# Kernel tuning notes

Hardware: AMD Instinct MI355X
Metric: run time of the kernel (lower is better)

The kernel has to match this reference:

```python
import jax, jax.numpy as jnp
import numpy as np

N_GROUPS = 4


def setup_inputs() -> dict:
    key = jax.random.key(0)
    ks = jax.random.split(key, 6)
    I, J, B = 512, 512, 4  # query tokens, key tokens, grid batch (B = 1 * n_groups)
    n_dim, out_per_group = 128, 4  # n_heads // n_groups = 16 // 4
    grid_q = jax.random.normal(ks[0], (I, 3), dtype=jnp.float32)
    grid_kv = jax.random.normal(ks[1], (B, J, 3), dtype=jnp.float32)
    W1 = jax.random.normal(ks[2], (3, n_dim), dtype=jnp.float32) * (1.0 / np.sqrt(3))
    b1 = jnp.zeros((n_dim,), dtype=jnp.float32)
    W2 = jax.random.normal(ks[3], (n_dim, n_dim), dtype=jnp.float32) * (1.0 / np.sqrt(n_dim))
    b2 = jnp.zeros((n_dim,), dtype=jnp.float32)
    W3 = jax.random.normal(ks[4], (n_dim, out_per_group), dtype=jnp.float32) * (1.0 / np.sqrt(n_dim))
    b3 = jnp.zeros((out_per_group,), dtype=jnp.float32)
    return {"grid_q": grid_q, "grid_kv": grid_kv, "W1": W1, "b1": b1,
            "W2": W2, "b2": b2, "W3": W3, "b3": b3}


def reference(grid_q, grid_kv, W1, b1, W2, b2, W3, b3):
    # grid_q: [I, 3] -> [1, I, 3]; grid_kv: [B, J, 3]
    gq = grid_q[None, :, :]
    # pairwise position difference: [B, I, J, 3]
    pos = gq[:, :, None, :] - grid_kv[:, None, :, :]
    # sign-log transform
    bias = jnp.sign(pos) * jnp.log1p(jnp.abs(pos))
    # tiny MLP: 3 -> n_dim -> n_dim -> heads//groups, pointwise over (B, I, J)
    h = jax.nn.relu(jnp.einsum('bijc,cd->bijd', bias, W1) + b1)
    h = jax.nn.relu(jnp.einsum('bijd,de->bije', h, W2) + b2)
    out = jnp.einsum('bije,eo->bijo', h, W3) + b3  # [B, I, J, O]
    # rearrange '(b g) i j o -> b (g o) i j' with g = N_GROUPS
    B, I, J, O = out.shape
    out = out.reshape(B // N_GROUPS, N_GROUPS, I, J, O)
    out = jnp.transpose(out, (0, 1, 4, 2, 3)).reshape(B // N_GROUPS, N_GROUPS * O, I, J)
    return out
```

## Files before the change

kernel.cpp:

```cpp
#include <hip/hip_runtime.h>
#include <math.h>

#define NDIM 128
#define TILE 64
#define NBLOCKS 1024
#define THREADS 512
#define POS_PER_BLOCK 1024
#define ITERS 16
#define CH 512

typedef __attribute__((ext_vector_type(8)))  short  short8;
typedef __attribute__((ext_vector_type(16))) float  float16;

__device__ __forceinline__ unsigned cvt_pk(float lo, float hi) {
    unsigned r;
    asm("v_cvt_pk_bf16_f32 %0, %1, %2" : "=v"(r) : "v"(lo), "v"(hi));
    return r;
}

__device__ __forceinline__ int kmap(int c, int jj) {
    return 32 * (c >> 2) + 16 * ((c >> 1) & 1) + 4 * (c & 1) + ((jj >> 2) << 3) + (jj & 3);
}

__global__ __launch_bounds__(512, 4)
void crpb_mfma7(const float* __restrict__ gq,
                const float* __restrict__ gkv,
                const float* __restrict__ W1,
                const float* __restrict__ b1,
                const float* __restrict__ W2,
                const float* __restrict__ b2,
                const float* __restrict__ W3,
                const float* __restrict__ b3,
                float* __restrict__ out)
{
    __shared__ __align__(16) unsigned short ash[2][16 * CH];
    __shared__ __align__(16) float red[2][4 * 4 * 64];

    const int tid  = threadIdx.x;
    const int lane = tid & 63;
    const int w    = __builtin_amdgcn_readfirstlane(tid >> 6);
    const int l31  = lane & 31;
    const int lh   = lane >> 5;

    const int ct = w & 3;
    const int ph = w >> 2;

    float16 b1cv, b2cv;
    #pragma unroll
    for (int q = 0; q < 16; ++q) {
        const int row = (q & 3) + 8 * (q >> 2) + 4 * lh;
        b1cv[q] = b1[ct * 32 + row];
        b2cv[q] = b2[ct * 32 + row];
    }

    short8 w1f;
    {
        const int ch = ct * 32 + l31;
        const float w0 = W1[ch], w1v = W1[128 + ch], w2v = W1[256 + ch];
        const unsigned u0 = cvt_pk(w0, w0), u1 = cvt_pk(w1v, w1v), u2 = cvt_pk(w2v, w2v);
        const float w0h = __uint_as_float(u0 << 16);
        const float w1h = __uint_as_float(u1 << 16);
        const float w2h = __uint_as_float(u2 << 16);
        const float w0l = w0 - w0h, w1l = w1v - w1h, w2l = w2v - w2h;
        unsigned d[4];
        if (lh == 0) {
            d[0] = cvt_pk(w0h, w0l);
            d[1] = cvt_pk(w0h, w1h);
            d[2] = cvt_pk(w1l, w1h);
            d[3] = cvt_pk(w2h, w2l);
        } else {
            d[0] = cvt_pk(w2h, 0.0f);
            d[1] = 0; d[2] = 0; d[3] = 0;
        }
        __builtin_memcpy(&w1f, d, 16);
    }

    short8 a2f[8];
    #pragma unroll
    for (int ks = 0; ks < 8; ++ks) {
        const int c = 2 * ks + lh;
        unsigned t0[4];
        #pragma unroll
        for (int t = 0; t < 4; ++t) {
            const int d0 = kmap(c, 2 * t), d1 = d0 + 1;
            t0[t] = cvt_pk(W2[d0 * 128 + ct * 32 + l31], W2[d1 * 128 + ct * 32 + l31]);
        }
        __builtin_memcpy(&a2f[ks], t0, 16);
    }

    short8 w3a[2];
    #pragma unroll
    for (int m = 0; m < 2; ++m) {
        unsigned tt[4];
        #pragma unroll
        for (int t = 0; t < 4; ++t) {
            const int chl = ((2 * t) & 3) + 8 * ((2 * t) >> 2) + 4 * lh + 16 * m;
            const int ch0 = ct * 32 + chl, ch1 = ch0 + 1;
            const float lo = (l31 < 4) ? W3[ch0 * 4 + l31] : 0.0f;
            const float hi = (l31 < 4) ? W3[ch1 * 4 + l31] : 0.0f;
            tt[t] = cvt_pk(lo, hi);
        }
        __builtin_memcpy(&w3a[m], tt, 16);
    }
    const float b3r = b3[(tid >> 6) & 3];

    const int posblock = blockIdx.x * POS_PER_BLOCK;
    const int bb = posblock >> 18;
    const float* kvrow = gkv + (size_t)(bb << 9) * 3;

    int ii = (posblock >> 9) & 511;
    float q0 = gq[ii * 3 + 0], q1 = gq[ii * 3 + 1], q2 = gq[ii * 3 + 2];
    const int pofs = ph * 32 + l31;
    const float* kp = kvrow + (size_t)((posblock & 511) + pofs) * 3;
    float kv0 = kp[0], kv1 = kp[1], kv2 = kp[2];

    auto phaseA = [&](int x, int buf) {
        const float c0 = q0 - kv0, c1 = q1 - kv1, c2 = q2 - kv2;
        const int pn = posblock + (((x + 1) & 15) << 6);
        const int iN = (pn >> 9) & 511, jN = pn & 511;
        q0 = gq[iN * 3 + 0]; q1 = gq[iN * 3 + 1]; q2 = gq[iN * 3 + 2];
        const float* kn = kvrow + (size_t)(jN + pofs) * 3;
        kv0 = kn[0]; kv1 = kn[1]; kv2 = kn[2];

        const float f0 = copysignf(__logf(1.0f + fabsf(c0)), c0);
        const float f1 = copysignf(__logf(1.0f + fabsf(c1)), c1);
        const float f2 = copysignf(__logf(1.0f + fabsf(c2)), c2);

        const unsigned u0 = cvt_pk(f0, f0), u1 = cvt_pk(f1, f1), u2 = cvt_pk(f2, f2);
        const float f0h = __uint_as_float(u0 << 16);
        const float f1h = __uint_as_float(u1 << 16);
        const float f2h = __uint_as_float(u2 << 16);
        const float f0l = f0 - f0h, f1l = f1 - f1h, f2l = f2 - f2h;

        unsigned d[4];
        if (lh == 0) {
            d[0] = u0;
            d[1] = cvt_pk(f0l, f1);
            d[2] = cvt_pk(f1, f1l);
            d[3] = u2;
        } else {
            d[0] = cvt_pk(f2l, 0.0f);
            d[1] = 0; d[2] = 0; d[3] = 0;
        }
        short8 bf; __builtin_memcpy(&bf, d, 16);

        float16 c1r = __builtin_amdgcn_mfma_f32_32x32x16_bf16(w1f, bf, b1cv, 0, 0, 0);

        unsigned pk0[4], pk1[4];
        #pragma unroll
        for (int t = 0; t < 4; ++t) {
            pk0[t] = cvt_pk(fmaxf(c1r[2 * t], 0.f),     fmaxf(c1r[2 * t + 1], 0.f));
            pk1[t] = cvt_pk(fmaxf(c1r[8 + 2 * t], 0.f), fmaxf(c1r[8 + 2 * t + 1], 0.f));
        }
        short8 v0, v1;
        __builtin_memcpy(&v0, pk0, 16);
        __builtin_memcpy(&v1, pk1, 16);
        *(short8*)&ash[buf][(4 * ct + lh) * CH + pofs * 8]     = v0;
        *(short8*)&ash[buf][(4 * ct + 2 + lh) * CH + pofs * 8] = v1;
    };

    phaseA(0, 0);
    __syncthreads();

    for (int it = 0; it < ITERS; ++it) {
        const int buf = it & 1;
        const int posbase = posblock + it * TILE;
        const int i  = (posbase >> 9) & 511;
        const int jb = posbase & 511;

        const unsigned short* br = &ash[buf][lh * CH + (ph * 32 + l31) * 8];
        short8 bfrag0 = *(const short8*)(br);
        float16 acc = __builtin_amdgcn_mfma_f32_32x32x16_bf16(a2f[0], bfrag0, b2cv, 0, 0, 0);
        #pragma unroll
        for (int ks = 1; ks < 8; ++ks) {
            short8 bfrag = *(const short8*)(br + ks * 2 * CH);
            acc = __builtin_amdgcn_mfma_f32_32x32x16_bf16(a2f[ks], bfrag, acc, 0, 0, 0);
        }

        {
            unsigned pk0[4], pk1[4];
            #pragma unroll
            for (int t = 0; t < 4; ++t) {
                pk0[t] = cvt_pk(fmaxf(acc[2 * t], 0.f),     fmaxf(acc[2 * t + 1], 0.f));
                pk1[t] = cvt_pk(fmaxf(acc[8 + 2 * t], 0.f), fmaxf(acc[8 + 2 * t + 1], 0.f));
            }
            short8 bm0, bm1;
            __builtin_memcpy(&bm0, pk0, 16);
            __builtin_memcpy(&bm1, pk1, 16);
            float16 p;
            #pragma unroll
            for (int r = 0; r < 16; ++r) p[r] = 0.0f;
            p = __builtin_amdgcn_mfma_f32_32x32x16_bf16(w3a[0], bm0, p, 0, 0, 0);
            p = __builtin_amdgcn_mfma_f32_32x32x16_bf16(w3a[1], bm1, p, 0, 0, 0);
            if (lh == 0) {
                #pragma unroll
                for (int o = 0; o < 4; ++o)
                    red[buf][(ct * 4 + o) * 64 + ph * 32 + l31] = p[o];
            }
        }

        if (it != ITERS - 1) phaseA(it + 1, 1 - buf);

        __syncthreads();

        if (tid < 256) {
            const int o = tid >> 6, pos = tid & 63;
            const float* rb = &red[buf][o * 64 + pos];
            const float v = b3r + rb[0] + rb[256] + rb[512] + rb[768];
            out[((size_t)((bb << 2) + o) << 18) + ((size_t)i << 9) + jb + pos] = v;
        }
    }
}

extern "C" void kernel_launch(void* const* d_in, const int* in_sizes, int n_in,
                              void* d_out, int out_size, void* d_ws, size_t ws_size,
                              hipStream_t stream) {
    const float* gq  = (const float*)d_in[0];
    const float* gkv = (const float*)d_in[1];
    const float* W1  = (const float*)d_in[2];
    const float* b1  = (const float*)d_in[3];
    const float* W2  = (const float*)d_in[4];
    const float* b2  = (const float*)d_in[5];
    const float* W3  = (const float*)d_in[6];
    const float* b3  = (const float*)d_in[7];
    float* out = (float*)d_out;

    crpb_mfma7<<<NBLOCKS, THREADS, 0, stream>>>(gq, gkv, W1, b1, W2, b2, W3, b3, out);
}
```

Before: 125.7 us.

## Give each wave two channel tiles, halve block size, fold b1 into MFMA

Blocks shrink from 512 to 256 threads, and each wave now computes two 32-channel tiles of the hidden layer. One B fragment read from LDS therefore feeds two MFMAs, and the cross-wave reduction drops from four partial sums to two. b1 is folded into the first-layer MFMA as an extra K column with input 1.0 (hi/lo split), which frees the bias accumulator registers. b2 is staged in LDS and reloaded each iteration. Each block now covers a single query row, so query coordinates are loaded once. The cost is higher per-wave register pressure (two sets of W2 fragments), with occupancy bounds lowered to 3.

```diff
diff --git a/kernel.cpp b/kernel.cpp
--- a/kernel.cpp
+++ b/kernel.cpp
@@ -1,15 +1,15 @@
 #include <hip/hip_runtime.h>
 #include <math.h>
 
-#define NDIM 128
+#define NBLOCKS 2048
+#define THREADS 256
 #define TILE 64
-#define NBLOCKS 1024
-#define THREADS 512
-#define POS_PER_BLOCK 1024
-#define ITERS 16
+#define POS_PER_BLOCK 512
+#define ITERS 8
 #define CH 512
 
 typedef __attribute__((ext_vector_type(8)))  short  short8;
+typedef __attribute__((ext_vector_type(4)))  float  float4v;
 typedef __attribute__((ext_vector_type(16))) float  float16;
 
 __device__ __forceinline__ unsigned cvt_pk(float lo, float hi) {
@@ -22,8 +22,8 @@
     return 32 * (c >> 2) + 16 * ((c >> 1) & 1) + 4 * (c & 1) + ((jj >> 2) << 3) + (jj & 3);
 }
 
-__global__ __launch_bounds__(512, 4)
-void crpb_mfma7(const float* __restrict__ gq,
+__global__ __launch_bounds__(256, 3)
+void crpb_mfma8(const float* __restrict__ gq,
                 const float* __restrict__ gkv,
                 const float* __restrict__ W1,
                 const float* __restrict__ b1,
@@ -34,7 +34,8 @@
                 float* __restrict__ out)
 {
     __shared__ __align__(16) unsigned short ash[2][16 * CH];
-    __shared__ __align__(16) float red[2][4 * 4 * 64];
+    __shared__ __align__(16) float red[2][2 * 4 * 64];
+    __shared__ __align__(16) float b2s[128];
 
     const int tid  = threadIdx.x;
     const int lane = tid & 63;
@@ -42,26 +43,26 @@
     const int l31  = lane & 31;
     const int lh   = lane >> 5;
 
-    const int ct = w & 3;
-    const int ph = w >> 2;
-
-    float16 b1cv, b2cv;
-    #pragma unroll
-    for (int q = 0; q < 16; ++q) {
-        const int row = (q & 3) + 8 * (q >> 2) + 4 * lh;
-        b1cv[q] = b1[ct * 32 + row];
-        b2cv[q] = b2[ct * 32 + row];
-    }
-
-    short8 w1f;
-    {
-        const int ch = ct * 32 + l31;
-        const float w0 = W1[ch], w1v = W1[128 + ch], w2v = W1[256 + ch];
-        const unsigned u0 = cvt_pk(w0, w0), u1 = cvt_pk(w1v, w1v), u2 = cvt_pk(w2v, w2v);
-        const float w0h = __uint_as_float(u0 << 16);
-        const float w1h = __uint_as_float(u1 << 16);
-        const float w2h = __uint_as_float(u2 << 16);
-        const float w0l = w0 - w0h, w1l = w1v - w1h, w2l = w2v - w2h;
+    if (tid < 128) b2s[tid] = b2[tid];
+
+    const int ct2 = w & 1;
+    const int ph  = w >> 1;
+    const int pofs = ph * 32 + l31;
+
+    float16 z16;
+    #pragma unroll
+    for (int r = 0; r < 16; ++r) z16[r] = 0.0f;
+
+    short8 w1f[2];
+    #pragma unroll
+    for (int mt = 0; mt < 2; ++mt) {
+        const int ch = (ct2 * 2 + mt) * 32 + l31;
+        const float w0 = W1[ch], w1v = W1[128 + ch], w2v = W1[256 + ch], b1v = b1[ch];
+        const float w0h = __uint_as_float(cvt_pk(w0, w0) << 16);
+        const float w1h = __uint_as_float(cvt_pk(w1v, w1v) << 16);
+        const float w2h = __uint_as_float(cvt_pk(w2v, w2v) << 16);
+        const float b1h = __uint_as_float(cvt_pk(b1v, b1v) << 16);
+        const float w0l = w0 - w0h, w1l = w1v - w1h, w2l = w2v - w2h, b1l = b1v - b1h;
         unsigned d[4];
         if (lh == 0) {
             d[0] = cvt_pk(w0h, w0l);
@@ -69,66 +70,69 @@
             d[2] = cvt_pk(w1l, w1h);
             d[3] = cvt_pk(w2h, w2l);
         } else {
-            d[0] = cvt_pk(w2h, 0.0f);
-            d[1] = 0; d[2] = 0; d[3] = 0;
-        }
-        __builtin_memcpy(&w1f, d, 16);
-    }
-
-    short8 a2f[8];
-    #pragma unroll
-    for (int ks = 0; ks < 8; ++ks) {
-        const int c = 2 * ks + lh;
-        unsigned t0[4];
-        #pragma unroll
-        for (int t = 0; t < 4; ++t) {
-            const int d0 = kmap(c, 2 * t), d1 = d0 + 1;
-            t0[t] = cvt_pk(W2[d0 * 128 + ct * 32 + l31], W2[d1 * 128 + ct * 32 + l31]);
-        }
-        __builtin_memcpy(&a2f[ks], t0, 16);
-    }
-
-    short8 w3a[2];
-    #pragma unroll
-    for (int m = 0; m < 2; ++m) {
-        unsigned tt[4];
-        #pragma unroll
-        for (int t = 0; t < 4; ++t) {
-            const int chl = ((2 * t) & 3) + 8 * ((2 * t) >> 2) + 4 * lh + 16 * m;
-            const int ch0 = ct * 32 + chl, ch1 = ch0 + 1;
-            const float lo = (l31 < 4) ? W3[ch0 * 4 + l31] : 0.0f;
-            const float hi = (l31 < 4) ? W3[ch1 * 4 + l31] : 0.0f;
-            tt[t] = cvt_pk(lo, hi);
-        }
-        __builtin_memcpy(&w3a[m], tt, 16);
-    }
-    const float b3r = b3[(tid >> 6) & 3];
+            d[0] = cvt_pk(w2h, b1h);
+            d[1] = cvt_pk(b1l, 0.0f);
+            d[2] = 0; d[3] = 0;
+        }
+        __builtin_memcpy(&w1f[mt], d, 16);
+    }
+
+    short8 a2f[2][8];
+    #pragma unroll
+    for (int mt = 0; mt < 2; ++mt) {
+        const int e = ct2 * 64 + mt * 32 + l31;
+        #pragma unroll
+        for (int ks = 0; ks < 8; ++ks) {
+            const int c = 2 * ks + lh;
+            unsigned t0[4];
+            #pragma unroll
+            for (int t = 0; t < 4; ++t) {
+                const int d0 = kmap(c, 2 * t), d1 = d0 + 1;
+                t0[t] = cvt_pk(W2[d0 * 128 + e], W2[d1 * 128 + e]);
+            }
+            __builtin_memcpy(&a2f[mt][ks], t0, 16);
+        }
+    }
+
+    short8 w3a[2][2];
+    #pragma unroll
+    for (int mt = 0; mt < 2; ++mt) {
+        #pragma unroll
+        for (int m2 = 0; m2 < 2; ++m2) {
+            unsigned tt[4];
+            #pragma unroll
+            for (int t = 0; t < 4; ++t) {
+                const int chl = ((2 * t) & 3) + 8 * ((2 * t) >> 2) + 4 * lh + 16 * m2;
+                const int ch0 = (ct2 * 2 + mt) * 32 + chl, ch1 = ch0 + 1;
+                const float lo = (l31 < 4) ? W3[ch0 * 4 + l31] : 0.0f;
+                const float hi = (l31 < 4) ? W3[ch1 * 4 + l31] : 0.0f;
+                tt[t] = cvt_pk(lo, hi);
+            }
+            __builtin_memcpy(&w3a[mt][m2], tt, 16);
+        }
+    }
+    const float b3r = b3[w];
 
     const int posblock = blockIdx.x * POS_PER_BLOCK;
     const int bb = posblock >> 18;
+    const int i  = (posblock >> 9) & 511;
+    const float q0 = gq[i * 3 + 0], q1 = gq[i * 3 + 1], q2 = gq[i * 3 + 2];
     const float* kvrow = gkv + (size_t)(bb << 9) * 3;
 
-    int ii = (posblock >> 9) & 511;
-    float q0 = gq[ii * 3 + 0], q1 = gq[ii * 3 + 1], q2 = gq[ii * 3 + 2];
-    const int pofs = ph * 32 + l31;
-    const float* kp = kvrow + (size_t)((posblock & 511) + pofs) * 3;
+    const float* kp = kvrow + (size_t)pofs * 3;
     float kv0 = kp[0], kv1 = kp[1], kv2 = kp[2];
 
     auto phaseA = [&](int x, int buf) {
         const float c0 = q0 - kv0, c1 = q1 - kv1, c2 = q2 - kv2;
-        const int pn = posblock + (((x + 1) & 15) << 6);
-        const int iN = (pn >> 9) & 511, jN = pn & 511;
-        q0 = gq[iN * 3 + 0]; q1 = gq[iN * 3 + 1]; q2 = gq[iN * 3 + 2];
-        const float* kn = kvrow + (size_t)(jN + pofs) * 3;
+        const float* kn = kvrow + (size_t)((((x + 1) & 7) << 6) + pofs) * 3;
         kv0 = kn[0]; kv1 = kn[1]; kv2 = kn[2];
 
         const float f0 = copysignf(__logf(1.0f + fabsf(c0)), c0);
         const float f1 = copysignf(__logf(1.0f + fabsf(c1)), c1);
         const float f2 = copysignf(__logf(1.0f + fabsf(c2)), c2);
-
-        const unsigned u0 = cvt_pk(f0, f0), u1 = cvt_pk(f1, f1), u2 = cvt_pk(f2, f2);
+        const unsigned u0 = cvt_pk(f0, f0), u2 = cvt_pk(f2, f2);
         const float f0h = __uint_as_float(u0 << 16);
-        const float f1h = __uint_as_float(u1 << 16);
+        const float f1h = __uint_as_float(cvt_pk(f1, f1) << 16);
         const float f2h = __uint_as_float(u2 << 16);
         const float f0l = f0 - f0h, f1l = f1 - f1h, f2l = f2 - f2h;
 
@@ -139,24 +143,28 @@
             d[2] = cvt_pk(f1, f1l);
             d[3] = u2;
         } else {
-            d[0] = cvt_pk(f2l, 0.0f);
-            d[1] = 0; d[2] = 0; d[3] = 0;
+            d[0] = cvt_pk(f2l, 1.0f);
+            d[1] = cvt_pk(1.0f, 0.0f);
+            d[2] = 0; d[3] = 0;
         }
         short8 bf; __builtin_memcpy(&bf, d, 16);
 
-        float16 c1r = __builtin_amdgcn_mfma_f32_32x32x16_bf16(w1f, bf, b1cv, 0, 0, 0);
-
-        unsigned pk0[4], pk1[4];
-        #pragma unroll
-        for (int t = 0; t < 4; ++t) {
-            pk0[t] = cvt_pk(fmaxf(c1r[2 * t], 0.f),     fmaxf(c1r[2 * t + 1], 0.f));
-            pk1[t] = cvt_pk(fmaxf(c1r[8 + 2 * t], 0.f), fmaxf(c1r[8 + 2 * t + 1], 0.f));
-        }
-        short8 v0, v1;
-        __builtin_memcpy(&v0, pk0, 16);
-        __builtin_memcpy(&v1, pk1, 16);
-        *(short8*)&ash[buf][(4 * ct + lh) * CH + pofs * 8]     = v0;
-        *(short8*)&ash[buf][(4 * ct + 2 + lh) * CH + pofs * 8] = v1;
+        #pragma unroll
+        for (int mt = 0; mt < 2; ++mt) {
+            const int cti = ct2 * 2 + mt;
+            float16 c1r = __builtin_amdgcn_mfma_f32_32x32x16_bf16(w1f[mt], bf, z16, 0, 0, 0);
+            unsigned pk0[4], pk1[4];
+            #pragma unroll
+            for (int t = 0; t < 4; ++t) {
+                pk0[t] = cvt_pk(fmaxf(c1r[2 * t], 0.f),     fmaxf(c1r[2 * t + 1], 0.f));
+                pk1[t] = cvt_pk(fmaxf(c1r[8 + 2 * t], 0.f), fmaxf(c1r[8 + 2 * t + 1], 0.f));
+            }
+            short8 v0, v1;
+            __builtin_memcpy(&v0, pk0, 16);
+            __builtin_memcpy(&v1, pk1, 16);
+            *(short8*)&ash[buf][(4 * cti + lh) * CH + pofs * 8]     = v0;
+            *(short8*)&ash[buf][(4 * cti + 2 + lh) * CH + pofs * 8] = v1;
+        }
     };
 
     phaseA(0, 0);
@@ -164,38 +172,45 @@
 
     for (int it = 0; it < ITERS; ++it) {
         const int buf = it & 1;
-        const int posbase = posblock + it * TILE;
-        const int i  = (posbase >> 9) & 511;
-        const int jb = posbase & 511;
-
-        const unsigned short* br = &ash[buf][lh * CH + (ph * 32 + l31) * 8];
-        short8 bfrag0 = *(const short8*)(br);
-        float16 acc = __builtin_amdgcn_mfma_f32_32x32x16_bf16(a2f[0], bfrag0, b2cv, 0, 0, 0);
-        #pragma unroll
-        for (int ks = 1; ks < 8; ++ks) {
+        const int jb = it * TILE;
+
+        float16 acc0, acc1;
+        #pragma unroll
+        for (int qr = 0; qr < 4; ++qr) {
+            float4v i0 = *(const float4v*)&b2s[(ct2 * 2 + 0) * 32 + 8 * qr + 4 * lh];
+            float4v i1 = *(const float4v*)&b2s[(ct2 * 2 + 1) * 32 + 8 * qr + 4 * lh];
+            #pragma unroll
+            for (int t = 0; t < 4; ++t) { acc0[4 * qr + t] = i0[t]; acc1[4 * qr + t] = i1[t]; }
+        }
+        const unsigned short* br = &ash[buf][lh * CH + pofs * 8];
+        #pragma unroll
+        for (int ks = 0; ks < 8; ++ks) {
             short8 bfrag = *(const short8*)(br + ks * 2 * CH);
-            acc = __builtin_amdgcn_mfma_f32_32x32x16_bf16(a2f[ks], bfrag, acc, 0, 0, 0);
+            acc0 = __builtin_amdgcn_mfma_f32_32x32x16_bf16(a2f[0][ks], bfrag, acc0, 0, 0, 0);
+            acc1 = __builtin_amdgcn_mfma_f32_32x32x16_bf16(a2f[1][ks], bfrag, acc1, 0, 0, 0);
         }
 
         {
-            unsigned pk0[4], pk1[4];
-            #pragma unroll
-            for (int t = 0; t < 4; ++t) {
-                pk0[t] = cvt_pk(fmaxf(acc[2 * t], 0.f),     fmaxf(acc[2 * t + 1], 0.f));
-                pk1[t] = cvt_pk(fmaxf(acc[8 + 2 * t], 0.f), fmaxf(acc[8 + 2 * t + 1], 0.f));
-            }
-            short8 bm0, bm1;
-            __builtin_memcpy(&bm0, pk0, 16);
-            __builtin_memcpy(&bm1, pk1, 16);
+            unsigned pa0[4], pa1[4], pb0[4], pb1[4];
+            #pragma unroll
+            for (int t = 0; t < 4; ++t) {
+                pa0[t] = cvt_pk(fmaxf(acc0[2 * t], 0.f),     fmaxf(acc0[2 * t + 1], 0.f));
+                pa1[t] = cvt_pk(fmaxf(acc0[8 + 2 * t], 0.f), fmaxf(acc0[8 + 2 * t + 1], 0.f));
+                pb0[t] = cvt_pk(fmaxf(acc1[2 * t], 0.f),     fmaxf(acc1[2 * t + 1], 0.f));
+                pb1[t] = cvt_pk(fmaxf(acc1[8 + 2 * t], 0.f), fmaxf(acc1[8 + 2 * t + 1], 0.f));
+            }
+            short8 fa0, fa1, fb0, fb1;
+            __builtin_memcpy(&fa0, pa0, 16); __builtin_memcpy(&fa1, pa1, 16);
+            __builtin_memcpy(&fb0, pb0, 16); __builtin_memcpy(&fb1, pb1, 16);
             float16 p;
-            #pragma unroll
-            for (int r = 0; r < 16; ++r) p[r] = 0.0f;
-            p = __builtin_amdgcn_mfma_f32_32x32x16_bf16(w3a[0], bm0, p, 0, 0, 0);
-            p = __builtin_amdgcn_mfma_f32_32x32x16_bf16(w3a[1], bm1, p, 0, 0, 0);
+            p = __builtin_amdgcn_mfma_f32_32x32x16_bf16(w3a[0][0], fa0, z16, 0, 0, 0);
+            p = __builtin_amdgcn_mfma_f32_32x32x16_bf16(w3a[0][1], fa1, p, 0, 0, 0);
+            p = __builtin_amdgcn_mfma_f32_32x32x16_bf16(w3a[1][0], fb0, p, 0, 0, 0);
+            p = __builtin_amdgcn_mfma_f32_32x32x16_bf16(w3a[1][1], fb1, p, 0, 0, 0);
             if (lh == 0) {
                 #pragma unroll
                 for (int o = 0; o < 4; ++o)
-                    red[buf][(ct * 4 + o) * 64 + ph * 32 + l31] = p[o];
+                    red[buf][ct2 * 256 + o * 64 + pofs] = p[o];
             }
         }
 
@@ -203,10 +218,9 @@
 
         __syncthreads();
 
-        if (tid < 256) {
-            const int o = tid >> 6, pos = tid & 63;
-            const float* rb = &red[buf][o * 64 + pos];
-            const float v = b3r + rb[0] + rb[256] + rb[512] + rb[768];
+        {
+            const int o = w, pos = lane;
+            const float v = b3r + red[buf][o * 64 + pos] + red[buf][256 + o * 64 + pos];
             out[((size_t)((bb << 2) + o) << 18) + ((size_t)i << 9) + jb + pos] = v;
         }
     }
@@ -225,5 +239,5 @@
     const float* b3  = (const float*)d_in[7];
     float* out = (float*)d_out;
 
-    crpb_mfma7<<<NBLOCKS, THREADS, 0, stream>>>(gq, gkv, W1, b1, W2, b2, W3, b3, out);
-}
+    crpb_mfma8<<<NBLOCKS, THREADS, 0, stream>>>(gq, gkv, W1, b1, W2, b2, W3, b3, out);
+}
```

After: 122.2 us. -2.8%, faster.
